# Kernel optimization log

Hardware: AMD Instinct MI355X
Metric: run time of the kernel (lower is better)

## Reference

```python
import jax, jax.numpy as jnp
import numpy as np

VOXEL_SIZE = 0.4
H, W = 512, 1408
FOOT = jnp.array([-1.0, 0.0, 1.0], dtype=jnp.float32)  # 3x3 splat footprint
NUSC_FREQ = np.array([1163161, 2309034, 188743, 2997643, 20317180, 852476, 243808, 2457947, 497017, 2731022, 7224789, 214411435, 5565043, 63191967, 76098082, 128860031, 141625221, 2307405309], np.float64)


def setup_inputs() -> dict:
    key = jax.random.key(0)
    k1, k2, k3 = jax.random.split(key, 3)
    B, NC = 1, 6
    X, Y, Z, C = 200, 200, 16, 17
    voxel_feats = jax.random.normal(k1, (B, X, Y, Z, C), jnp.float32)
    density = jax.random.uniform(k2, (B, X, Y, Z, 1), jnp.float32)
    # regular voxel-center grid (get_presudo_xyz)
    pc_min = np.array([-40.0, -40.0, -1.0])
    xs = pc_min[0] + (np.arange(X) + 0.5) * VOXEL_SIZE
    ys = pc_min[1] + (np.arange(Y) + 0.5) * VOXEL_SIZE
    zs = pc_min[2] + (np.arange(Z) + 0.5) * VOXEL_SIZE
    Xg, Yg, Zg = np.meshgrid(xs, ys, zs, indexing='ij')
    pc_xyz = jnp.asarray(np.stack([Xg, Yg, Zg], -1).reshape(-1, 3), dtype=jnp.float32)
    # plausible world-to-camera extrinsics: identity rotation, scene pushed to depth ~50
    vm = np.tile(np.eye(4, dtype=np.float32), (B, NC, 1, 1))
    vm[..., 2, 3] = 50.0
    vm[:, :, 0, 3] = np.linspace(-2.0, 2.0, NC, dtype=np.float32)
    viewmats = jnp.asarray(vm)
    Kc = np.zeros((B, NC, 3, 3), np.float32)
    Kc[..., 0, 0] = 560.0; Kc[..., 1, 1] = 560.0
    Kc[..., 0, 2] = W / 2.0; Kc[..., 1, 2] = H / 2.0; Kc[..., 2, 2] = 1.0
    Ks = jnp.asarray(Kc)
    gt_sem = jax.random.randint(k3, (B, NC, H, W), 0, 17, dtype=jnp.int32)
    class_weights = jnp.asarray(1.0 / np.log(NUSC_FREQ[:17] + 0.001), jnp.float32)
    return dict(voxel_feats=voxel_feats, density=density, viewmats=viewmats, Ks=Ks,
                gt_sem=gt_sem, pc_xyz=pc_xyz, class_weights=class_weights)


def _render(viewmat, Kmat, xyz, feats, opac):
    """Differentiable gaussian splat onto an HxW feature image (additive compositing)."""
    R, t = viewmat[:3, :3], viewmat[:3, 3]
    p = xyz @ R.T + t                      # [N,3] camera space
    z = jnp.maximum(p[:, 2], 1e-3)
    fx, fy, cx, cy = Kmat[0, 0], Kmat[1, 1], Kmat[0, 2], Kmat[1, 2]
    u = fx * p[:, 0] / z + cx
    v = fy * p[:, 1] / z + cy
    s2 = VOXEL_SIZE * VOXEL_SIZE           # isotropic scale^2 (regular-grid KDTree dists)
    j00, j11 = fx / z, fy / z              # EWA projection Jacobian
    j02 = -fx * p[:, 0] / (z * z)
    j12 = -fy * p[:, 1] / (z * z)
    a = s2 * (j00 * j00 + j02 * j02) + 0.3  # 2D covariance + 0.3 pixel dilation (3DGS)
    b = s2 * (j02 * j12)
    c = s2 * (j11 * j11 + j12 * j12) + 0.3
    det = a * c - b * b
    ca, cb, cc = c / det, -b / det, a / det  # conic (inverse 2D covariance)
    px = jnp.round(u)[:, None, None] + FOOT[None, :, None]   # [N,3,3]
    py = jnp.round(v)[:, None, None] + FOOT[None, None, :]
    ddx = px - u[:, None, None]
    ddy = py - v[:, None, None]
    g = jnp.exp(-0.5 * (ca[:, None, None] * ddx * ddx
                        + 2.0 * cb[:, None, None] * ddx * ddy
                        + cc[:, None, None] * ddy * ddy))
    valid = ((p[:, 2] > 0.1)[:, None, None]
             & (px >= 0) & (px < W) & (py >= 0) & (py < H))
    wgt = jnp.where(valid, opac[:, None, None] * g, 0.0)     # [N,3,3]
    idx = (jnp.clip(py, 0, H - 1) * W + jnp.clip(px, 0, W - 1)).astype(jnp.int32).reshape(-1)
    contrib = (wgt[..., None] * feats[:, None, None, :]).reshape(-1, feats.shape[-1])
    return jax.ops.segment_sum(contrib, idx, num_segments=H * W)  # [H*W, C]


def reference(voxel_feats, density, viewmats, Ks, gt_sem, pc_xyz, class_weights):
    B, NC = voxel_feats.shape[0], viewmats.shape[1]
    C = voxel_feats.shape[-1]
    loss_b = jnp.float32(0.0)
    for b in range(B):
        feats = voxel_feats[b].reshape(-1, C)
        opac = density[b].reshape(-1)
        loss_c = jnp.float32(0.0)
        for cid in range(NC):
            logits = _render(viewmats[b, cid], Ks[b, cid], pc_xyz, feats, opac)
            gt = gt_sem[b, cid].reshape(-1)
            logp = jax.nn.log_softmax(logits, axis=-1)
            nll = -jnp.take_along_axis(logp, gt[:, None], axis=1)[:, 0]
            # masked, class-weighted CE, matching nn.CrossEntropyLoss(weight, 'mean')
            wvec = jnp.where(gt != 0, class_weights[gt], 0.0)
            loss_c = loss_c + jnp.sum(wvec * nll) / jnp.maximum(jnp.sum(wvec), 1e-8)
        loss_b = loss_b + loss_c / NC
    return loss_b / B  # gaussian_sem_weight = 1.0
```

## Files before the change

### kernel.cpp

```cpp
#include <hip/hip_runtime.h>
#include <hip/hip_fp16.h>

#define HH 512
#define WW 1408
#define HWPIX (HH*WW)
#define HALFPIX (HWPIX/2)
#define NCH 17
#define NX 200
#define NY 200
#define NZ 16
#define NVOX (NX*NY*NZ)
#define NCAM 6
#define VOXSZ 0.4f
#define PCMINX (-40.0f)
#define PCMINY (-40.0f)
#define PCMINZ (-1.0f)
#define TIX 20
#define NPREP_T (NY*10)
#define LDSF_STRIDE 276
#define L2E 1.44269504f
#define NBLK2 (HALFPIX/256)
#define XP2 (NBLK2/8)

union U4H8 { uint4 u; __half2 h2[4]; __half h[8]; };

__global__ __launch_bounds__(256) void prep_kernel(
    const float* __restrict__ feats,
    const float* __restrict__ density,
    const float* __restrict__ viewmats,
    const float* __restrict__ Ks,
    uint4*  __restrict__ h4tab,
    __half* __restrict__ h1tab,
    float4* __restrict__ xtab,
    float4* __restrict__ ytab,
    unsigned int* __restrict__ pxany,
    float* __restrict__ accum)
{
    const int t = threadIdx.x;
    if (blockIdx.x < NPREP_T) {
        __shared__ float ldsF[TIX * LDSF_STRIDE];
        __shared__ float ldsD[TIX][NZ];
        const int iy     = blockIdx.x / 10;
        const int ixBase = (blockIdx.x % 10) * TIX;
        for (int q = t; q < TIX * 68; q += 256) {
            const int r = q / 68, j4 = q % 68;
            const float4 v = *reinterpret_cast<const float4*>(
                feats + ((size_t)(ixBase + r) * NY + iy) * 272 + j4 * 4);
            *reinterpret_cast<float4*>(&ldsF[r * LDSF_STRIDE + j4 * 4]) = v;
        }
        for (int q = t; q < TIX * 4; q += 256) {
            const int r = q / 4, jd = q % 4;
            const float4 v = *reinterpret_cast<const float4*>(
                density + ((size_t)(ixBase + r) * NY + iy) * NZ + jd * 4);
            *reinterpret_cast<float4*>(&ldsD[r][jd * 4]) = v;
        }
        __syncthreads();
        for (int q = t; q < TIX * NZ * 2; q += 256) {
            const int kg = q & 1;
            const int r  = (q >> 1) % TIX;
            const int iz = q / (2 * TIX);
            const float d = ldsD[r][iz];
            const int jb = r * LDSF_STRIDE + iz * NCH + kg * 8;
            U4H8 pk;
            #pragma unroll
            for (int i = 0; i < 8; ++i) pk.h[i] = __float2half(ldsF[jb + i] * d);
            h4tab[((size_t)(iz * NY + iy) * NX + ixBase + r) * 2 + kg] = pk.u;
        }
        for (int q = t; q < NZ * (TIX / 2); q += 256) {
            const int rp = (q % (TIX / 2)) * 2;
            const int iz = q / (TIX / 2);
            __half2 hv;
            hv.x = __float2half(ldsF[rp * LDSF_STRIDE + iz * NCH + 16] * ldsD[rp][iz]);
            hv.y = __float2half(ldsF[(rp + 1) * LDSF_STRIDE + iz * NCH + 16] * ldsD[rp + 1][iz]);
            *reinterpret_cast<__half2*>(
                &h1tab[(size_t)(iz * NY + iy) * NX + ixBase + rp]) = hv;
        }
        return;
    }

    const int bid = blockIdx.x - NPREP_T;
    if (bid == 0 && t < 16) accum[t] = 0.f;

    const int cam = bid / NZ;
    const int iz  = bid % NZ;
    const float* vm = viewmats + cam * 16;
    const float* K  = Ks + cam * 9;
    const float fx = K[0], fy = K[4], cx = K[2], cy = K[5];
    const float zw = PCMINZ + ((float)iz + 0.5f) * VOXSZ;
    const float pz = vm[10] * zw + vm[11];
    const bool layerok = pz > 0.1f;
    const float z = fmaxf(pz, 0.001f);
    const float invz = 1.0f / z;
    const float sk  = VOXSZ * invz;
    const float A0x = (VOXSZ * fx * invz) * (VOXSZ * fx * invz);
    const float A0y = (VOXSZ * fy * invz) * (VOXSZ * fy * invz);
    const float S0C = sqrtf(0.5f * L2E);

    for (int px = t; px < WW; px += blockDim.x) {
        const float xt = ((float)px - cx) * z / fx - vm[3];
        const int ixe = (int)rintf((xt - PCMINX) * 2.5f - 0.5f);
        int sel = -1; float usel = 0.f;
        for (int d = -1; d <= 1; ++d) {
            const int ix = ixe + d;
            const float xw = PCMINX + ((float)ix + 0.5f) * VOXSZ;
            const float pxc = vm[0] * xw + vm[3];
            const float u = fx * pxc * invz + cx;
            if (ix >= 0 && ix < NX && fabsf((float)px - rintf(u)) <= 1.0f) {
                sel = ix; usel = u;
            }
        }
        float4 e;
        if (sel >= 0 && layerok) {
            const float gx = cx - usel;
            const float sx = sk * gx;
            e = make_float4(((float)px - usel) * S0C, sx,
                            fmaf(sx, sx, A0x + 0.3f), __int_as_float(sel));
        } else {
            e = make_float4(0.f, 0.f, 1.f, __int_as_float(-1));
        }
        xtab[(cam * NZ + iz) * WW + px] = e;
    }
    for (int py = t; py < HH; py += blockDim.x) {
        const float yt = ((float)py - cy) * z / fy - vm[7];
        const int iye = (int)rintf((yt - PCMINY) * 2.5f - 0.5f);
        int sel = -1; float vsel = 0.f;
        for (int d = -1; d <= 1; ++d) {
            const int iy = iye + d;
            const float yw = PCMINY + ((float)iy + 0.5f) * VOXSZ;
            const float pyc = vm[5] * yw + vm[7];
            const float v = fy * pyc * invz + cy;
            if (iy >= 0 && iy < NY && fabsf((float)py - rintf(v)) <= 1.0f) {
                sel = iy; vsel = v;
            }
        }
        float4 e;
        if (sel >= 0 && layerok) {
            const float gy = cy - vsel;
            const float sy = sk * gy;
            e = make_float4(((float)py - vsel) * S0C, sy,
                            fmaf(sy, sy, A0y + 0.3f), __int_as_float(sel * NX));
        } else {
            e = make_float4(0.f, 0.f, 1.f, __int_as_float(-1));
        }
        ytab[(cam * NZ + iz) * HH + py] = e;
    }

    if (iz == 0) {
        for (int px = t; px < WW; px += blockDim.x) {
            unsigned int any = 0;
            for (int z2 = 0; z2 < NZ; ++z2) {
                const float zw2 = PCMINZ + ((float)z2 + 0.5f) * VOXSZ;
                const float pz2 = vm[10] * zw2 + vm[11];
                if (pz2 <= 0.1f) continue;
                const float zz  = fmaxf(pz2, 0.001f);
                const float iv  = 1.0f / zz;
                const float xt  = ((float)px - cx) * zz / fx - vm[3];
                const int ixe = (int)rintf((xt - PCMINX) * 2.5f - 0.5f);
                for (int d = -1; d <= 1; ++d) {
                    const int ix = ixe + d;
                    const float xw = PCMINX + ((float)ix + 0.5f) * VOXSZ;
                    const float u = fx * (vm[0] * xw + vm[3]) * iv + cx;
                    if (ix >= 0 && ix < NX && fabsf((float)px - rintf(u)) <= 1.0f)
                        any = 1;
                }
            }
            pxany[cam * WW + px] = any;
        }
    }
}

#define STAGE(IZ, XE, YE, Pp0, Pp1, Pfs, Pwv)                                 \
    {                                                                         \
        const int izOff = (IZ) * (NY * NX);                                   \
        const int ix = __float_as_int(XE.w);                                  \
        const float x1 = XE.x * XE.x;                                         \
        _Pragma("unroll")                                                     \
        for (int p = 0; p < 2; ++p) {                                         \
            const float4 ye = YE[p];                                          \
            const int iyNX = __float_as_int(ye.w);                            \
            if (__builtin_amdgcn_readfirstlane(iyNX) >= 0) {                  \
                const bool cov = ix >= 0;                                     \
                const float bb  = XE.y * ye.y;                                \
                const float det = fmaf(-bb, bb, XE.z * ye.z);                 \
                float num = fmaf(ye.z, x1, XE.z * (ye.x * ye.x));             \
                num = fmaf(XE.x * ye.x, -(bb + bb), num);                     \
                const float w = __builtin_amdgcn_exp2f(-num * __builtin_amdgcn_rcpf(det)); \
                Pwv[p] = cov ? w : 0.f;                                       \
                if (cov) {                                                    \
                    const int vi = izOff + iyNX + ix;                         \
                    const size_t h4i = (size_t)vi * 2;                        \
                    Pp0[p] = h4tab[h4i];                                      \
                    Pp1[p] = h4tab[h4i + 1];                                  \
                    Pfs[p] = h1tab[vi];                                       \
                }                                                             \
            } else {                                                          \
                Pwv[p] = 0.f;                                                 \
            }                                                                 \
        }                                                                     \
    }

#define CONSUME(Pp0, Pp1, Pfs, Pwv)                                           \
    {                                                                         \
        _Pragma("unroll")                                                     \
        for (int p = 0; p < 2; ++p) {                                         \
            if (Pwv[p] > 0.f) {                                               \
                const __half2 wh = __float2half2_rn(Pwv[p]);                  \
                U4H8 q0, q1; q0.u = Pp0[p]; q1.u = Pp1[p];                    \
                _Pragma("unroll")                                             \
                for (int i = 0; i < 4; ++i) {                                 \
                    acc2[p][i]   = __hfma2(wh, q0.h2[i], acc2[p][i]);         \
                    acc2[p][4+i] = __hfma2(wh, q1.h2[i], acc2[p][4+i]);       \
                }                                                             \
                acc16[p] = fmaf(Pwv[p], __half2float(Pfs[p]), acc16[p]);      \
            }                                                                 \
        }                                                                     \
    }

__global__ __launch_bounds__(256) void gather_loss_kernel(
    const uint4*  __restrict__ h4tab,
    const __half* __restrict__ h1tab,
    const float4* __restrict__ xtab,
    const float4* __restrict__ ytab,
    const unsigned int* __restrict__ pxany,
    const int*    __restrict__ gt,
    const float*  __restrict__ cw,
    float* __restrict__ accum)
{
    const int b    = blockIdx.x;
    const int xcd  = b & 7;
    const int slot = b >> 3;
    const int cam  = slot % 6;
    const int xloc = slot / 6;
    const int pixT = (xcd * XP2 + xloc) * 256 + threadIdx.x;
    const int pixB = pixT + HALFPIX;

    const int rowT = pixT / WW;
    const int px   = pixT - rowT * WW;
    const int pyT  = __builtin_amdgcn_readfirstlane(rowT);
    const int pyB  = pyT + 256;

    const int gT = gt[(size_t)cam * HWPIX + pixT];
    const int gB = gt[(size_t)cam * HWPIX + pixB];
    const float cwT = cw[gT];
    const float cwB = cw[gB];

    __half2 acc2[2][8];
    float acc16[2] = {0.f, 0.f};
    #pragma unroll
    for (int p = 0; p < 2; ++p)
        #pragma unroll
        for (int i = 0; i < 8; ++i) acc2[p][i] = __float2half2_rn(0.f);

    const unsigned int cany = pxany[cam * WW + px];
    const bool live = __any((int)(cany != 0));
    if (live) {
        const float4* xb  = xtab + (size_t)(cam * NZ) * WW + px;
        const float4* ybT = ytab + (size_t)(cam * NZ) * HH + pyT;
        const float4* ybB = ytab + (size_t)(cam * NZ) * HH + pyB;

        uint4 Ap0[2], Ap1[2]; __half Afs[2]; float Awv[2];
        uint4 Bp0[2], Bp1[2]; __half Bfs[2]; float Bwv[2];
        float4 txA, txB, yeA[2], yeB[2];
        float4 txC, txD, yeC[2], yeD[2];

        txA = xb[0];  yeA[0] = ybT[0];  yeA[1] = ybB[0];
        txB = xb[WW]; yeB[0] = ybT[HH]; yeB[1] = ybB[HH];
        txC = xb[2 * WW]; yeC[0] = ybT[2 * HH]; yeC[1] = ybB[2 * HH];
        txD = xb[3 * WW]; yeD[0] = ybT[3 * HH]; yeD[1] = ybB[3 * HH];

        STAGE(0, txA, yeA, Ap0, Ap1, Afs, Awv);
        STAGE(1, txB, yeB, Bp0, Bp1, Bfs, Bwv);

        #pragma unroll
        for (int iz = 2; iz < NZ; iz += 2) {
            txA = txC; yeA[0] = yeC[0]; yeA[1] = yeC[1];
            txB = txD; yeB[0] = yeD[0]; yeB[1] = yeD[1];
            if (iz + 2 < NZ) {
                txC = xb[(size_t)(iz + 2) * WW];
                yeC[0] = ybT[(size_t)(iz + 2) * HH];
                yeC[1] = ybB[(size_t)(iz + 2) * HH];
                txD = xb[(size_t)(iz + 3) * WW];
                yeD[0] = ybT[(size_t)(iz + 3) * HH];
                yeD[1] = ybB[(size_t)(iz + 3) * HH];
            }

            CONSUME(Ap0, Ap1, Afs, Awv);
            STAGE(iz, txA, yeA, Ap0, Ap1, Afs, Awv);
            CONSUME(Bp0, Bp1, Bfs, Bwv);
            STAGE(iz + 1, txB, yeB, Bp0, Bp1, Bfs, Bwv);
        }
        CONSUME(Ap0, Ap1, Afs, Awv);
        CONSUME(Bp0, Bp1, Bfs, Bwv);
    }

    const int gsel[2] = {gT, gB};
    const float cws[2] = {cwT, cwB};
    float wnll = 0.f, wsum = 0.f;
    #pragma unroll
    for (int p = 0; p < 2; ++p) {
        const int g = gsel[p];
        const float wvt = (g != 0) ? cws[p] : 0.f;
        float nll;
        if (live) {
            float accf[NCH];
            #pragma unroll
            for (int i = 0; i < 8; ++i) {
                const float2 f2v = __half22float2(acc2[p][i]);
                accf[2*i + 0] = f2v.x;
                accf[2*i + 1] = f2v.y;
            }
            accf[16] = acc16[p];

            float m = accf[0];
            #pragma unroll
            for (int k = 1; k < NCH; ++k) m = fmaxf(m, accf[k]);
            const float mL = m * L2E;
            float s = 0.f;
            #pragma unroll
            for (int k = 0; k < NCH; ++k)
                s += __builtin_amdgcn_exp2f(fmaf(accf[k], L2E, -mL));
            const float lse = m + 0.69314718f * __builtin_amdgcn_logf(s);

            float selLogit = 0.f;
            #pragma unroll
            for (int k = 0; k < NCH; ++k)
                selLogit = (g == k) ? accf[k] : selLogit;
            nll = lse - selLogit;
        } else {
            nll = 0.69314718f * __builtin_amdgcn_logf(17.0f);
        }
        wnll += wvt * nll;
        wsum += wvt;
    }

    #pragma unroll
    for (int off = 32; off > 0; off >>= 1) {
        wnll += __shfl_down(wnll, off);
        wsum += __shfl_down(wsum, off);
    }
    __shared__ float red[4][2];
    const int wave = threadIdx.x >> 6, lane = threadIdx.x & 63;
    if (lane == 0) { red[wave][0] = wnll; red[wave][1] = wsum; }
    __syncthreads();
    if (threadIdx.x < 2) {
        const float v = red[0][threadIdx.x] + red[1][threadIdx.x] +
                        red[2][threadIdx.x] + red[3][threadIdx.x];
        atomicAdd(&accum[cam * 2 + threadIdx.x], v);
    }
}

__global__ void finalize_kernel(const float* __restrict__ accum, float* __restrict__ out)
{
    if (threadIdx.x == 0 && blockIdx.x == 0) {
        float loss = 0.f;
        for (int c = 0; c < NCAM; ++c)
            loss += accum[c * 2 + 0] / fmaxf(accum[c * 2 + 1], 1e-8f);
        out[0] = loss / (float)NCAM;
    }
}

extern "C" void kernel_launch(void* const* d_in, const int* in_sizes, int n_in,
                              void* d_out, int out_size, void* d_ws, size_t ws_size,
                              hipStream_t stream)
{
    const float* voxel_feats = (const float*)d_in[0];
    const float* density     = (const float*)d_in[1];
    const float* viewmats    = (const float*)d_in[2];
    const float* Ks          = (const float*)d_in[3];
    const int*   gt_sem      = (const int*)  d_in[4];
    const float* pc_xyz      = (const float*)d_in[5];  (void)pc_xyz;
    const float* cw          = (const float*)d_in[6];
    float* out = (float*)d_out;

    char* w = (char*)d_ws;
    float*        accum = (float*)w;                    w += 256;
    unsigned int* pxany = (unsigned int*)w;             w += ((size_t)NCAM * WW * sizeof(unsigned int) + 255) & ~255ULL;
    float4* xtab  = (float4*)w;                         w += (size_t)NCAM * NZ * WW * sizeof(float4);
    float4* ytab  = (float4*)w;                         w += (size_t)NCAM * NZ * HH * sizeof(float4);
    uint4*  h4tab = (uint4*)w;                          w += (size_t)2 * NVOX * sizeof(uint4);
    __half* h1tab = (__half*)w;

    prep_kernel<<<NPREP_T + NCAM * NZ, 256, 0, stream>>>(
        voxel_feats, density, viewmats, Ks, h4tab, h1tab,
        xtab, ytab, pxany, accum);

    gather_loss_kernel<<<NBLK2 * NCAM, 256, 0, stream>>>(h4tab, h1tab, xtab, ytab,
                                                         pxany, gt_sem, cw, accum);
    finalize_kernel<<<1, 64, 0, stream>>>(accum, out);
}
```

Before: 242.7 us.

## Store voxel tables in source (x,y,z) order and drop LDS transpose in prep

After: 247.5 us. +2.0%, slower.

```diff
diff --git a/kernel.cpp b/kernel.cpp
--- a/kernel.cpp
+++ b/kernel.cpp
@@ -15,9 +15,7 @@
 #define PCMINX (-40.0f)
 #define PCMINY (-40.0f)
 #define PCMINZ (-1.0f)
-#define TIX 20
-#define NPREP_T (NY*10)
-#define LDSF_STRIDE 276
+#define NPREP_C 625
 #define L2E 1.44269504f
 #define NBLK2 (HALFPIX/256)
 #define XP2 (NBLK2/8)
@@ -37,48 +35,45 @@
     float* __restrict__ accum)
 {
     const int t = threadIdx.x;
-    if (blockIdx.x < NPREP_T) {
-        __shared__ float ldsF[TIX * LDSF_STRIDE];
-        __shared__ float ldsD[TIX][NZ];
-        const int iy     = blockIdx.x / 10;
-        const int ixBase = (blockIdx.x % 10) * TIX;
-        for (int q = t; q < TIX * 68; q += 256) {
-            const int r = q / 68, j4 = q % 68;
-            const float4 v = *reinterpret_cast<const float4*>(
-                feats + ((size_t)(ixBase + r) * NY + iy) * 272 + j4 * 4);
-            *reinterpret_cast<float4*>(&ldsF[r * LDSF_STRIDE + j4 * 4]) = v;
-        }
-        for (int q = t; q < TIX * 4; q += 256) {
-            const int r = q / 4, jd = q % 4;
-            const float4 v = *reinterpret_cast<const float4*>(
-                density + ((size_t)(ixBase + r) * NY + iy) * NZ + jd * 4);
-            *reinterpret_cast<float4*>(&ldsD[r][jd * 4]) = v;
-        }
-        __syncthreads();
-        for (int q = t; q < TIX * NZ * 2; q += 256) {
-            const int kg = q & 1;
-            const int r  = (q >> 1) % TIX;
-            const int iz = q / (2 * TIX);
-            const float d = ldsD[r][iz];
-            const int jb = r * LDSF_STRIDE + iz * NCH + kg * 8;
-            U4H8 pk;
-            #pragma unroll
-            for (int i = 0; i < 8; ++i) pk.h[i] = __float2half(ldsF[jb + i] * d);
-            h4tab[((size_t)(iz * NY + iy) * NX + ixBase + r) * 2 + kg] = pk.u;
-        }
-        for (int q = t; q < NZ * (TIX / 2); q += 256) {
-            const int rp = (q % (TIX / 2)) * 2;
-            const int iz = q / (TIX / 2);
-            __half2 hv;
-            hv.x = __float2half(ldsF[rp * LDSF_STRIDE + iz * NCH + 16] * ldsD[rp][iz]);
-            hv.y = __float2half(ldsF[(rp + 1) * LDSF_STRIDE + iz * NCH + 16] * ldsD[rp + 1][iz]);
-            *reinterpret_cast<__half2*>(
-                &h1tab[(size_t)(iz * NY + iy) * NX + ixBase + rp]) = hv;
-        }
+    if (blockIdx.x < NPREP_C) {
+        const int tau = blockIdx.x * 256 + t;
+        const int c   = tau >> 2;
+        const int q   = tau & 3;
+        float f[68];
+        const float* src = feats + (size_t)c * 272 + q * 68;
+        #pragma unroll
+        for (int k = 0; k < 17; ++k)
+            *reinterpret_cast<float4*>(&f[k * 4]) =
+                *reinterpret_cast<const float4*>(src + k * 4);
+        const float4 dv = *reinterpret_cast<const float4*>(
+            density + (size_t)c * NZ + q * 4);
+        const float dd[4] = {dv.x, dv.y, dv.z, dv.w};
+
+        uint4 outv[8];
+        #pragma unroll
+        for (int izl = 0; izl < 4; ++izl) {
+            #pragma unroll
+            for (int kg = 0; kg < 2; ++kg) {
+                U4H8 pk;
+                #pragma unroll
+                for (int i = 0; i < 8; ++i)
+                    pk.h[i] = __float2half(f[izl * 17 + kg * 8 + i] * dd[izl]);
+                outv[izl * 2 + kg] = pk.u;
+            }
+        }
+        uint4* dst = h4tab + ((size_t)c * NZ + q * 4) * 2;
+        #pragma unroll
+        for (int k = 0; k < 8; ++k) dst[k] = outv[k];
+
+        union { uint2 u; __half h[4]; } hh;
+        #pragma unroll
+        for (int izl = 0; izl < 4; ++izl)
+            hh.h[izl] = __float2half(f[izl * 17 + 16] * dd[izl]);
+        *reinterpret_cast<uint2*>(h1tab + (size_t)c * NZ + q * 4) = hh.u;
         return;
     }
 
-    const int bid = blockIdx.x - NPREP_T;
+    const int bid = blockIdx.x - NPREP_C;
     if (bid == 0 && t < 16) accum[t] = 0.f;
 
     const int cam = bid / NZ;
@@ -138,7 +133,7 @@
             const float gy = cy - vsel;
             const float sy = sk * gy;
             e = make_float4(((float)py - vsel) * S0C, sy,
-                            fmaf(sy, sy, A0y + 0.3f), __int_as_float(sel * NX));
+                            fmaf(sy, sy, A0y + 0.3f), __int_as_float(sel));
         } else {
             e = make_float4(0.f, 0.f, 1.f, __int_as_float(-1));
         }
@@ -171,14 +166,14 @@
 
 #define STAGE(IZ, XE, YE, Pp0, Pp1, Pfs, Pwv)                                 \
     {                                                                         \
-        const int izOff = (IZ) * (NY * NX);                                   \
         const int ix = __float_as_int(XE.w);                                  \
+        const int ixNY = ix * NY;                   \
         const float x1 = XE.x * XE.x;                                         \
         _Pragma("unroll")                                                     \
         for (int p = 0; p < 2; ++p) {                                         \
             const float4 ye = YE[p];                                          \
-            const int iyNX = __float_as_int(ye.w);                            \
-            if (__builtin_amdgcn_readfirstlane(iyNX) >= 0) {                  \
+            const int iyv = __float_as_int(ye.w);                             \
+            if (__builtin_amdgcn_readfirstlane(iyv) >= 0) {                   \
                 const bool cov = ix >= 0;                                     \
                 const float bb  = XE.y * ye.y;                                \
                 const float det = fmaf(-bb, bb, XE.z * ye.z);                 \
@@ -187,7 +182,7 @@
                 const float w = __builtin_amdgcn_exp2f(-num * __builtin_amdgcn_rcpf(det)); \
                 Pwv[p] = cov ? w : 0.f;                                       \
                 if (cov) {                                                    \
-                    const int vi = izOff + iyNX + ix;                         \
+                    const int vi = ((ixNY + iyv) << 4) + (IZ);                \
                     const size_t h4i = (size_t)vi * 2;                        \
                     Pp0[p] = h4tab[h4i];                                      \
                     Pp1[p] = h4tab[h4i + 1];                                  \
@@ -380,7 +375,7 @@
     uint4*  h4tab = (uint4*)w;                          w += (size_t)2 * NVOX * sizeof(uint4);
     __half* h1tab = (__half*)w;
 
-    prep_kernel<<<NPREP_T + NCAM * NZ, 256, 0, stream>>>(
+    prep_kernel<<<NPREP_C + NCAM * NZ, 256, 0, stream>>>(
         voxel_feats, density, viewmats, Ks, h4tab, h1tab,
         xtab, ytab, pxany, accum);
 
```
